# Optimization experiments

Hardware: AMD Instinct MI355X
Metric: run time of the kernel (lower is better)

Reference implementation:

```python
import jax, jax.numpy as jnp
import numpy as np
from jax import lax

SEGMENTS = 64
KERNEL = 5


def setup_inputs() -> dict:
    key = jax.random.key(0)
    k1, k2, k3 = jax.random.split(key, 3)
    B, S, F = 4, 4096, 1024
    A6 = 512 * 6
    inp = jax.random.normal(k1, (B, S, F), dtype=jnp.float32)
    W = jax.random.normal(k2, (A6, F), dtype=jnp.float32) * (1.0 / np.sqrt(F))
    b = jax.random.normal(k3, (A6,), dtype=jnp.float32) * 0.01
    return {"inp": inp, "W": W, "b": b}


def reference(inp, W, b):
    # Fused projection: [B,S,F] @ [F,6A] -> [B,S,6A]
    x = jnp.einsum('bsf,af->bsa', inp, W) + b
    qry, key, val, seg, loc, out = jnp.split(x, 6, axis=2)  # each [B,S,A]
    B, S, A = out.shape

    # Global aggregated attention branch
    agg = qry.mean(axis=1)                              # [B,A]
    scores = jnp.einsum('ba,bsa->bs', agg, key)         # [B,S]
    w = jax.nn.softmax(scores, axis=1)                  # [B,S]
    ctx = jnp.einsum('bs,bsa->ba', w, val)              # [B,A]
    aggregated = ctx[:, None, :] * out                  # [B,S,A]

    # Segment max-pool branch
    nseg = S // SEGMENTS
    seg4 = seg.reshape(B, nseg, SEGMENTS, A)
    seg_max = seg4.max(axis=2, keepdims=True)           # [B,nseg,1,A]
    segment_max_pooled = (seg_max * out.reshape(B, nseg, SEGMENTS, A)).reshape(B, S, A)

    # Local sliding-window max-pool branch (stride 1, pad KERNEL//2, -inf padding)
    pad = KERNEL // 2
    local_max_pooled = lax.reduce_window(
        loc, -jnp.inf, lax.max,
        window_dimensions=(1, KERNEL, 1),
        window_strides=(1, 1, 1),
        padding=((0, 0), (pad, pad), (0, 0)))           # [B,S,A]

    return aggregated + segment_max_pooled + local_max_pooled
```

## Files before the change

### kernel.cpp

```cpp
#include <hip/hip_runtime.h>
#include <hip/hip_bf16.h>
#include <stdint.h>

#define B_    4
#define S_    4096
#define F_    1024
#define A_    512
#define N3_   1536
#define M_    16384

#define BM    256
#define BN    192
#define BK    64
#define NT    (F_ / BK)

typedef __attribute__((ext_vector_type(8))) __bf16 bf16x8;
typedef __attribute__((ext_vector_type(4))) float  f32x4;

__device__ __forceinline__ float bflo(unsigned int u) {
  union { unsigned int i; float f; } v; v.i = u << 16; return v.f;
}
__device__ __forceinline__ float bfhi(unsigned int u) {
  union { unsigned int i; float f; } v; v.i = u & 0xffff0000u; return v.f;
}

__device__ __forceinline__ ushort4 cvt_bf4(float4 v) {
  ushort4 o;
  o.x = __builtin_bit_cast(unsigned short, __float2bfloat16(v.x));
  o.y = __builtin_bit_cast(unsigned short, __float2bfloat16(v.y));
  o.z = __builtin_bit_cast(unsigned short, __float2bfloat16(v.z));
  o.w = __builtin_bit_cast(unsigned short, __float2bfloat16(v.w));
  return o;
}

typedef __attribute__((address_space(3))) unsigned int lds_uint;
typedef const __attribute__((address_space(1))) unsigned int glob_uint;
__device__ __forceinline__ void lds_load16(const void* g, void* l) {
  __builtin_amdgcn_global_load_lds((glob_uint*)g, (lds_uint*)l, 16, 0, 0);
}

__global__ __launch_bounds__(256) void convert_mean_kernel(
    const float* __restrict__ inp, const float* __restrict__ W,
    unsigned short* __restrict__ inp_bf, unsigned short* __restrict__ w_bf,
    float* __restrict__ mu) {
  int blk = blockIdx.x;
  int t   = threadIdx.x;
  int r0  = blk * 32;
  int b   = r0 >> 12;
  float acc0 = 0.f, acc1 = 0.f, acc2 = 0.f, acc3 = 0.f;
  for (int r = 0; r < 32; r++) {
    size_t row = (size_t)(r0 + r);
    float4 v = ((const float4*)(inp + row * F_))[t];
    acc0 += v.x; acc1 += v.y; acc2 += v.z; acc3 += v.w;
    ((ushort4*)(inp_bf + row * F_))[t] = cvt_bf4(v);
  }
  atomicAdd(&mu[b * F_ + t * 4 + 0], acc0);
  atomicAdd(&mu[b * F_ + t * 4 + 1], acc1);
  atomicAdd(&mu[b * F_ + t * 4 + 2], acc2);
  atomicAdd(&mu[b * F_ + t * 4 + 3], acc3);

  const float* Wc = W + (size_t)N3_ * F_;
  const int n4 = (N3_ * F_) / 4;
  for (int i = blk * 256 + t; i < n4; i += 512 * 256) {
    ((ushort4*)w_bf)[i] = cvt_bf4(((const float4*)Wc)[i]);
  }
}

__global__ void agg_kernel(const float* __restrict__ mu, const float* __restrict__ W,
                           const float* __restrict__ bias, float* __restrict__ agg) {
  int gw = blockIdx.x * 4 + (threadIdx.x >> 6);
  int lane = threadIdx.x & 63;
  int b = gw >> 9, a = gw & 511;
  const float4* wr = (const float4*)(W + (size_t)a * F_);
  const float4* mr = (const float4*)(mu + b * F_);
  float s = 0.f;
#pragma unroll
  for (int k = 0; k < 4; k++) {
    float4 wv = wr[lane + 64 * k], mv = mr[lane + 64 * k];
    s += wv.x * mv.x + wv.y * mv.y + wv.z * mv.z + wv.w * mv.w;
  }
  for (int off = 32; off; off >>= 1) s += __shfl_down(s, off);
  if (lane == 0) agg[b * A_ + a] = s * (1.f / S_) + bias[a];
}

__global__ void v_kernel(const float* __restrict__ agg, const float* __restrict__ W,
                         const float* __restrict__ bias, float* __restrict__ v,
                         float* __restrict__ cvec) {
  int fc = blockIdx.x;
  int ac = blockIdx.y;
  int t = threadIdx.x;
  int f = fc * 256 + t;
  const float* Wk = W + (size_t)A_ * F_;
  float s0 = 0.f, s1 = 0.f, s2 = 0.f, s3 = 0.f;
  int a0 = ac * 64;
  for (int a = a0; a < a0 + 64; a++) {
    float wv = Wk[(size_t)a * F_ + f];
    s0 += agg[a] * wv;
    s1 += agg[A_ + a] * wv;
    s2 += agg[2 * A_ + a] * wv;
    s3 += agg[3 * A_ + a] * wv;
  }
  atomicAdd(&v[f], s0);
  atomicAdd(&v[F_ + f], s1);
  atomicAdd(&v[2 * F_ + f], s2);
  atomicAdd(&v[3 * F_ + f], s3);

  if (fc == 0 && ac == 0) {
    int bb = t >> 6, l = t & 63;
    float c = 0.f;
#pragma unroll
    for (int i = 0; i < 8; i++) c += agg[bb * A_ + l + 64 * i] * bias[A_ + l + 64 * i];
    for (int off = 32; off; off >>= 1) c += __shfl_down(c, off);
    if (l == 0) cvec[bb] = c;
  }
}

__global__ void scores_kernel(const unsigned short* __restrict__ inp_bf,
                              const float* __restrict__ v,
                              const float* __restrict__ cvec, float* __restrict__ scores) {
  int lane = threadIdx.x & 63;
  int row = blockIdx.x * 4 + (threadIdx.x >> 6);
  int b = row >> 12;
  const uint4* ip = (const uint4*)(inp_bf + (size_t)row * F_);
  const float4* vp = (const float4*)(v + b * F_);
  float s = 0.f;
#pragma unroll
  for (int k = 0; k < 2; k++) {
    uint4 x = ip[lane + 64 * k];
    float4 va = vp[(lane + 64 * k) * 2];
    float4 vb = vp[(lane + 64 * k) * 2 + 1];
    s += bflo(x.x) * va.x + bfhi(x.x) * va.y + bflo(x.y) * va.z + bfhi(x.y) * va.w +
         bflo(x.z) * vb.x + bfhi(x.z) * vb.y + bflo(x.w) * vb.z + bfhi(x.w) * vb.w;
  }
  for (int off = 32; off; off >>= 1) s += __shfl_down(s, off);
  if (lane == 0) scores[row] = s + cvec[b];
}

__global__ void softmax_kernel(float* __restrict__ sc) {
  __shared__ float red[256];
  int b = blockIdx.x, t = threadIdx.x;
  float* p = sc + b * S_;
  float vals[16];
  float m = -1e30f;
#pragma unroll
  for (int i = 0; i < 16; i++) { vals[i] = p[t + i * 256]; m = fmaxf(m, vals[i]); }
  red[t] = m; __syncthreads();
  for (int o = 128; o; o >>= 1) { if (t < o) red[t] = fmaxf(red[t], red[t + o]); __syncthreads(); }
  m = red[0]; __syncthreads();
  float sum = 0.f;
#pragma unroll
  for (int i = 0; i < 16; i++) { vals[i] = __expf(vals[i] - m); sum += vals[i]; }
  red[t] = sum; __syncthreads();
  for (int o = 128; o; o >>= 1) { if (t < o) red[t] += red[t + o]; __syncthreads(); }
  float inv = 1.f / red[0];
#pragma unroll
  for (int i = 0; i < 16; i++) p[t + i * 256] = vals[i] * inv;
}

__global__ void u_kernel(const unsigned short* __restrict__ inp_bf,
                         const float* __restrict__ w, float* __restrict__ u) {
  int b = blockIdx.z, fc = blockIdx.y, sc = blockIdx.x;
  int t = threadIdx.x;
  int f2 = fc * 512 + t * 2;
  int s0 = sc * 128;
  const float* wp = w + b * S_ + s0;
  const unsigned short* ip = inp_bf + ((size_t)(b * S_ + s0)) * F_ + f2;
  float a0 = 0.f, a1 = 0.f;
  for (int s = 0; s < 128; s++) {
    unsigned int xv = *(const unsigned int*)&ip[(size_t)s * F_];
    float ws = wp[s];
    a0 += ws * bflo(xv);
    a1 += ws * bfhi(xv);
  }
  atomicAdd(&u[b * F_ + f2], a0);
  atomicAdd(&u[b * F_ + f2 + 1], a1);
}

__global__ void ctx_kernel(const float* __restrict__ u, const float* __restrict__ W,
                           const float* __restrict__ bias, float* __restrict__ ctx) {
  int gw = blockIdx.x * 4 + (threadIdx.x >> 6);
  int lane = threadIdx.x & 63;
  int b = gw >> 9, a = gw & 511;
  const float4* wr = (const float4*)(W + (size_t)(2 * A_ + a) * F_);
  const float4* ur = (const float4*)(u + b * F_);
  float s = 0.f;
#pragma unroll
  for (int k = 0; k < 4; k++) {
    float4 wv = wr[lane + 64 * k], uv = ur[lane + 64 * k];
    s += wv.x * uv.x + wv.y * uv.y + wv.z * uv.z + wv.w * uv.w;
  }
  for (int off = 32; off; off >>= 1) s += __shfl_down(s, off);
  if (lane == 0) ctx[b * A_ + a] = s + bias[2 * A_ + a];
}

__global__ __launch_bounds__(512, 2) void gemm_kernel(
    const __hip_bfloat16* __restrict__ Abf,
    const __hip_bfloat16* __restrict__ Wbf,
    const float* __restrict__ bias,
    __hip_bfloat16* __restrict__ X) {
  extern __shared__ unsigned short smem[];
  unsigned short* ldsA = smem;
  unsigned short* ldsB = smem + 32768;

  int bid = blockIdx.x;
  int swz = (bid & 7) * 64 + (bid >> 3);
  int mb = swz >> 3;
  int nb = swz & 7;

  int tid  = threadIdx.x;
  int lane = tid & 63;
  int wv   = tid >> 6;
  int wm   = wv >> 2;
  int wn   = wv & 3;
  int lo   = lane & 15, hi = lane >> 4, sw = lane & 7;

  int bir0 = (((hi * 16)      ^ (sw << 4)) >> 1);
  int bir1 = (((64 + hi * 16) ^ (sw << 4)) >> 1);

  const __hip_bfloat16* Ab = Abf + (size_t)mb * BM * F_;
  const __hip_bfloat16* Bb = Wbf + (size_t)nb * BN * F_;

  int srow = tid >> 3;
  int sel  = ((tid & 7) ^ (srow & 7)) * 8;
  int ldst = wv * 512;

  f32x4 acc[8][3];
#pragma unroll
  for (int i = 0; i < 8; i++)
#pragma unroll
    for (int j = 0; j < 3; j++) acc[i][j] = (f32x4){0.f, 0.f, 0.f, 0.f};

  int aBase = (wm * 128 + lo) * 64;
  int bBase = (wn * 48 + lo) * 64;

#define STAGE(kt_, buf_)                                                                   \
  {                                                                                        \
    int kof_ = (kt_) * BK;                                                                 \
    unsigned short* la_ = ldsA + (buf_) * 16384;                                           \
    unsigned short* lb_ = ldsB + (buf_) * 12288;                                           \
    lds_load16(Ab + (size_t)(srow) * F_ + kof_ + sel,        la_ + 0 * 4096 + ldst);       \
    lds_load16(Ab + (size_t)(64 + srow) * F_ + kof_ + sel,   la_ + 1 * 4096 + ldst);       \
    lds_load16(Ab + (size_t)(128 + srow) * F_ + kof_ + sel,  la_ + 2 * 4096 + ldst);       \
    lds_load16(Ab + (size_t)(192 + srow) * F_ + kof_ + sel,  la_ + 3 * 4096 + ldst);       \
    lds_load16(Bb + (size_t)(srow) * F_ + kof_ + sel,        lb_ + 0 * 4096 + ldst);       \
    lds_load16(Bb + (size_t)(64 + srow) * F_ + kof_ + sel,   lb_ + 1 * 4096 + ldst);       \
    lds_load16(Bb + (size_t)(128 + srow) * F_ + kof_ + sel,  lb_ + 2 * 4096 + ldst);       \
  }

  STAGE(0, 0);

  for (int kt = 0; kt < NT; ++kt) {
    int c = kt & 1;
    __builtin_amdgcn_s_barrier();
    if (kt + 1 < NT) {
      STAGE(kt + 1, c ^ 1);
      asm volatile("s_waitcnt vmcnt(7)" ::: "memory");
    } else {
      asm volatile("s_waitcnt vmcnt(0)" ::: "memory");
    }
    __builtin_amdgcn_s_barrier();
    __builtin_amdgcn_sched_barrier(0);

    const unsigned short* la = ldsA + c * 16384;
    const unsigned short* lb = ldsB + c * 12288;

    bf16x8 aq[4][2], b01[2][2], b2[2];

#pragma unroll
    for (int i = 0; i < 4; i++) {
      aq[i][0] = *(const bf16x8*)&la[aBase + i * 1024 + bir0];
      aq[i][1] = *(const bf16x8*)&la[aBase + i * 1024 + bir1];
    }
#pragma unroll
    for (int j = 0; j < 2; j++) {
      b01[j][0] = *(const bf16x8*)&lb[bBase + j * 1024 + bir0];
      b01[j][1] = *(const bf16x8*)&lb[bBase + j * 1024 + bir1];
    }
    __builtin_amdgcn_s_setprio(1);
#pragma unroll
    for (int i = 0; i < 4; i++)
#pragma unroll
      for (int j = 0; j < 2; j++) {
        acc[i][j] = __builtin_amdgcn_mfma_f32_16x16x32_bf16(aq[i][0], b01[j][0], acc[i][j], 0, 0, 0);
        acc[i][j] = __builtin_amdgcn_mfma_f32_16x16x32_bf16(aq[i][1], b01[j][1], acc[i][j], 0, 0, 0);
      }
    __builtin_amdgcn_s_setprio(0);
    __builtin_amdgcn_sched_barrier(0);

    b2[0] = *(const bf16x8*)&lb[bBase + 2 * 1024 + bir0];
    b2[1] = *(const bf16x8*)&lb[bBase + 2 * 1024 + bir1];
    __builtin_amdgcn_s_setprio(1);
#pragma unroll
    for (int i = 0; i < 4; i++) {
      acc[i][2] = __builtin_amdgcn_mfma_f32_16x16x32_bf16(aq[i][0], b2[0], acc[i][2], 0, 0, 0);
      acc[i][2] = __builtin_amdgcn_mfma_f32_16x16x32_bf16(aq[i][1], b2[1], acc[i][2], 0, 0, 0);
    }
    __builtin_amdgcn_s_setprio(0);
    __builtin_amdgcn_sched_barrier(0);

#pragma unroll
    for (int i = 0; i < 4; i++) {
      aq[i][0] = *(const bf16x8*)&la[aBase + 4096 + i * 1024 + bir0];
      aq[i][1] = *(const bf16x8*)&la[aBase + 4096 + i * 1024 + bir1];
    }
    __builtin_amdgcn_s_setprio(1);
#pragma unroll
    for (int i = 0; i < 4; i++) {
      acc[4 + i][2] = __builtin_amdgcn_mfma_f32_16x16x32_bf16(aq[i][0], b2[0], acc[4 + i][2], 0, 0, 0);
      acc[4 + i][2] = __builtin_amdgcn_mfma_f32_16x16x32_bf16(aq[i][1], b2[1], acc[4 + i][2], 0, 0, 0);
    }
    __builtin_amdgcn_s_setprio(0);
    __builtin_amdgcn_sched_barrier(0);

    __builtin_amdgcn_s_setprio(1);
#pragma unroll
    for (int i = 0; i < 4; i++)
#pragma unroll
      for (int j = 0; j < 2; j++) {
        acc[4 + i][j] = __builtin_amdgcn_mfma_f32_16x16x32_bf16(aq[i][0], b01[j][0], acc[4 + i][j], 0, 0, 0);
        acc[4 + i][j] = __builtin_amdgcn_mfma_f32_16x16x32_bf16(aq[i][1], b01[j][1], acc[4 + i][j], 0, 0, 0);
      }
    __builtin_amdgcn_s_setprio(0);
    __builtin_amdgcn_sched_barrier(0);
  }
#undef STAGE

#pragma unroll
  for (int fm = 0; fm < 8; fm++) {
    int grow = mb * BM + wm * 128 + fm * 16 + hi * 4;
#pragma unroll
    for (int fn = 0; fn < 3; fn++) {
      int gcol = nb * BN + wn * 48 + fn * 16 + lo;
      float bv = bias[gcol];
#pragma unroll
      for (int rg = 0; rg < 4; rg++) {
        X[(size_t)(grow + rg) * N3_ + gcol] = __float2bfloat16(acc[fm][fn][rg] + bv);
      }
    }
  }
}

__global__ void final_kernel(const unsigned short* __restrict__ X,
                             const float* __restrict__ ctx,
                             float* __restrict__ out) {
  int b = blockIdx.y, seg = blockIdx.x;
  int t = threadIdx.x;
  int c0 = t * 2;
  int sbase = seg * 64;

  float m0 = -1e30f, m1 = -1e30f;
  size_t base = ((size_t)b * S_ + sbase) * N3_;
  for (int r = 0; r < 64; r++) {
    unsigned int sv = *(const unsigned int*)&X[base + (size_t)r * N3_ + c0];
    m0 = fmaxf(m0, bflo(sv));
    m1 = fmaxf(m1, bfhi(sv));
  }
  float2 cx = *(const float2*)&ctx[b * A_ + c0];
  float g0 = cx.x + m0, g1 = cx.y + m1;

  auto loadloc = [&](int s) -> unsigned int {
    if ((unsigned)s >= (unsigned)S_) return 0xFF80FF80u;
    return *(const unsigned int*)&X[((size_t)b * S_ + s) * N3_ + A_ + c0];
  };
  unsigned int w0 = loadloc(sbase - 2), w1 = loadloc(sbase - 1);
  unsigned int w2 = loadloc(sbase),     w3 = loadloc(sbase + 1);
  for (int rr = 0; rr < 64; rr++) {
    int s = sbase + rr;
    unsigned int w4 = loadloc(s + 2);
    float lo = fmaxf(fmaxf(fmaxf(bflo(w0), bflo(w1)), fmaxf(bflo(w2), bflo(w3))), bflo(w4));
    float hi = fmaxf(fmaxf(fmaxf(bfhi(w0), bfhi(w1)), fmaxf(bfhi(w2), bfhi(w3))), bfhi(w4));
    unsigned int ov = *(const unsigned int*)&X[((size_t)b * S_ + s) * N3_ + 2 * A_ + c0];
    float2 res;
    res.x = g0 * bflo(ov) + lo;
    res.y = g1 * bfhi(ov) + hi;
    *(float2*)&out[((size_t)b * S_ + s) * A_ + c0] = res;
    w0 = w1; w1 = w2; w2 = w3; w3 = w4;
  }
}

extern "C" void kernel_launch(void* const* d_in, const int* in_sizes, int n_in,
                              void* d_out, int out_size, void* d_ws, size_t ws_size,
                              hipStream_t stream) {
  const float* inp  = (const float*)d_in[0];
  const float* W    = (const float*)d_in[1];
  const float* bias = (const float*)d_in[2];
  float* out = (float*)d_out;
  char* ws = (char*)d_ws;

  const size_t X_OFF    = 0;
  const size_t INP_OFF  = 50331648;
  const size_t W_OFF    = 83886080;
  const size_t MU_OFF   = 87031808;
  const size_t U_OFF    = MU_OFF + 16384;
  const size_t V_OFF    = U_OFF + 16384;
  const size_t CV_OFF   = V_OFF + 16384;
  const size_t AGG_OFF  = CV_OFF + 256;
  const size_t CTX_OFF  = AGG_OFF + 8192;
  const size_t SC_OFF   = CTX_OFF + 8192;

  unsigned short* xbf    = (unsigned short*)(ws + X_OFF);
  unsigned short* inp_bf = (unsigned short*)(ws + INP_OFF);
  unsigned short* w_bf   = (unsigned short*)(ws + W_OFF);
  float* mu     = (float*)(ws + MU_OFF);
  float* u      = (float*)(ws + U_OFF);
  float* v      = (float*)(ws + V_OFF);
  float* cvec   = (float*)(ws + CV_OFF);
  float* agg    = (float*)(ws + AGG_OFF);
  float* ctx    = (float*)(ws + CTX_OFF);
  float* scores = (float*)(ws + SC_OFF);

  static int lds_attr_set = 0;
  (void)lds_attr_set;
  hipFuncSetAttribute(reinterpret_cast<const void*>(gemm_kernel),
                      hipFuncAttributeMaxDynamicSharedMemorySize, 114688);

  hipMemsetAsync(ws + MU_OFF, 0, 3 * 16384 + 256, stream);
  convert_mean_kernel<<<512, 256, 0, stream>>>(inp, W, inp_bf, w_bf, mu);
  gemm_kernel<<<512, 512, 114688, stream>>>((const __hip_bfloat16*)inp_bf,
                                            (const __hip_bfloat16*)w_bf,
                                            bias + 3 * A_, (__hip_bfloat16*)xbf);
  agg_kernel<<<512, 256, 0, stream>>>(mu, W, bias, agg);
  v_kernel<<<dim3(4, 8), 256, 0, stream>>>(agg, W, bias, v, cvec);
  scores_kernel<<<4096, 256, 0, stream>>>(inp_bf, v, cvec, scores);
  softmax_kernel<<<4, 256, 0, stream>>>(scores);
  u_kernel<<<dim3(32, 2, 4), 256, 0, stream>>>(inp_bf, scores, u);
  ctx_kernel<<<512, 256, 0, stream>>>(u, W, bias, ctx);
  final_kernel<<<dim3(64, 4), 256, 0, stream>>>(xbf, ctx, out);
}
```

Before: 151.3 us.

## Fuse pooling epilogue into GEMM and drop the intermediate X buffer

The GEMM now gives each block 64 columns from each of the seg, loc and out groups, so one block holds all three projections for its 256 rows. Segment max, the local sliding max and the final combine are computed in the epilogue through a transposed LDS tile, and fp32 output is written directly. This removes the bf16 X round trip through global memory and the separate final kernel. A small fixup kernel patches the sliding-window results at tile boundaries using side buffers, and the GEMM's warp tiling and load staging are reorganised.

```diff
diff --git a/kernel.cpp b/kernel.cpp
--- a/kernel.cpp
+++ b/kernel.cpp
@@ -10,9 +10,9 @@
 #define M_    16384
 
 #define BM    256
-#define BN    192
 #define BK    64
 #define NT    (F_ / BK)
+#define LDP   266
 
 typedef __attribute__((ext_vector_type(8))) __bf16 bf16x8;
 typedef __attribute__((ext_vector_type(4))) float  f32x4;
@@ -23,13 +23,16 @@
 __device__ __forceinline__ float bfhi(unsigned int u) {
   union { unsigned int i; float f; } v; v.i = u & 0xffff0000u; return v.f;
 }
+__device__ __forceinline__ float bf1(unsigned short u) {
+  union { unsigned int i; float f; } v; v.i = ((unsigned int)u) << 16; return v.f;
+}
+__device__ __forceinline__ unsigned short bfc(float f) {
+  return __builtin_bit_cast(unsigned short, __float2bfloat16(f));
+}
 
 __device__ __forceinline__ ushort4 cvt_bf4(float4 v) {
   ushort4 o;
-  o.x = __builtin_bit_cast(unsigned short, __float2bfloat16(v.x));
-  o.y = __builtin_bit_cast(unsigned short, __float2bfloat16(v.y));
-  o.z = __builtin_bit_cast(unsigned short, __float2bfloat16(v.z));
-  o.w = __builtin_bit_cast(unsigned short, __float2bfloat16(v.w));
+  o.x = bfc(v.x); o.y = bfc(v.y); o.z = bfc(v.z); o.w = bfc(v.w);
   return o;
 }
 
@@ -193,14 +196,19 @@
   if (lane == 0) ctx[b * A_ + a] = s + bias[2 * A_ + a];
 }
 
-__global__ __launch_bounds__(512, 2) void gemm_kernel(
+__global__ __launch_bounds__(512, 2) void gemm_fused(
     const __hip_bfloat16* __restrict__ Abf,
     const __hip_bfloat16* __restrict__ Wbf,
-    const float* __restrict__ bias,
-    __hip_bfloat16* __restrict__ X) {
+    const float* __restrict__ biasP,
+    const float* __restrict__ ctx,
+    float* __restrict__ out,
+    unsigned short* __restrict__ sideLoc,
+    float* __restrict__ sideGO) {
   extern __shared__ unsigned short smem[];
   unsigned short* ldsA = smem;
   unsigned short* ldsB = smem + 32768;
+  unsigned short* Xt   = smem;
+  float* segred = (float*)((char*)smem + 192 * LDP * 2);
 
   int bid = blockIdx.x;
   int swz = (bid & 7) * 64 + (bid >> 3);
@@ -210,171 +218,225 @@
   int tid  = threadIdx.x;
   int lane = tid & 63;
   int wv   = tid >> 6;
-  int wm   = wv >> 2;
-  int wn   = wv & 3;
+  int wm   = wv >> 1;
+  int wn   = wv & 1;
   int lo   = lane & 15, hi = lane >> 4, sw = lane & 7;
 
   int bir0 = (((hi * 16)      ^ (sw << 4)) >> 1);
   int bir1 = (((64 + hi * 16) ^ (sw << 4)) >> 1);
 
   const __hip_bfloat16* Ab = Abf + (size_t)mb * BM * F_;
-  const __hip_bfloat16* Bb = Wbf + (size_t)nb * BN * F_;
 
   int srow = tid >> 3;
   int sel  = ((tid & 7) ^ (srow & 7)) * 8;
   int ldst = wv * 512;
 
-  f32x4 acc[8][3];
-#pragma unroll
-  for (int i = 0; i < 8; i++)
-#pragma unroll
-    for (int j = 0; j < 3; j++) acc[i][j] = (f32x4){0.f, 0.f, 0.f, 0.f};
-
-  int aBase = (wm * 128 + lo) * 64;
-  int bBase = (wn * 48 + lo) * 64;
-
-#define STAGE(kt_, buf_)                                                                   \
-  {                                                                                        \
-    int kof_ = (kt_) * BK;                                                                 \
-    unsigned short* la_ = ldsA + (buf_) * 16384;                                           \
-    unsigned short* lb_ = ldsB + (buf_) * 12288;                                           \
-    lds_load16(Ab + (size_t)(srow) * F_ + kof_ + sel,        la_ + 0 * 4096 + ldst);       \
-    lds_load16(Ab + (size_t)(64 + srow) * F_ + kof_ + sel,   la_ + 1 * 4096 + ldst);       \
-    lds_load16(Ab + (size_t)(128 + srow) * F_ + kof_ + sel,  la_ + 2 * 4096 + ldst);       \
-    lds_load16(Ab + (size_t)(192 + srow) * F_ + kof_ + sel,  la_ + 3 * 4096 + ldst);       \
-    lds_load16(Bb + (size_t)(srow) * F_ + kof_ + sel,        lb_ + 0 * 4096 + ldst);       \
-    lds_load16(Bb + (size_t)(64 + srow) * F_ + kof_ + sel,   lb_ + 1 * 4096 + ldst);       \
-    lds_load16(Bb + (size_t)(128 + srow) * F_ + kof_ + sel,  lb_ + 2 * 4096 + ldst);       \
-  }
-
-  STAGE(0, 0);
+  f32x4 acc[4][6];
+#pragma unroll
+  for (int i = 0; i < 4; i++)
+#pragma unroll
+    for (int j = 0; j < 6; j++) acc[i][j] = (f32x4){0.f, 0.f, 0.f, 0.f};
+
+  int aBase = (wm * 64 + lo) * 64;
+  int bBase = (wn * 96 + lo) * 64;
+
+#define STG_A(kt_, buf_, r_)                                                              \
+  lds_load16(Ab + (size_t)((r_) * 64 + srow) * F_ + (kt_) * BK + sel,                     \
+             ldsA + (buf_) * 16384 + (r_) * 4096 + ldst)
+#define STG_B(kt_, buf_, q_)                                                              \
+  lds_load16(Wbf + (size_t)((q_) * 512 + nb * 64 + srow) * F_ + (kt_) * BK + sel,         \
+             ldsB + (buf_) * 12288 + (q_) * 4096 + ldst)
+
+  STG_A(0, 0, 0); STG_A(0, 0, 1); STG_A(0, 0, 2); STG_A(0, 0, 3);
+  STG_B(0, 0, 0); STG_B(0, 0, 1); STG_B(0, 0, 2);
 
   for (int kt = 0; kt < NT; ++kt) {
-    int c = kt & 1;
-    __builtin_amdgcn_s_barrier();
-    if (kt + 1 < NT) {
-      STAGE(kt + 1, c ^ 1);
-      asm volatile("s_waitcnt vmcnt(7)" ::: "memory");
+    int c = kt & 1, nx = c ^ 1;
+    bool pf = (kt + 1 < NT);
+    const unsigned short* la = ldsA + c * 16384;
+    const unsigned short* lb = ldsB + c * 12288;
+    bf16x8 af[4][2], bfr[2][2];
+
+    if (pf) {
+      STG_A(kt + 1, nx, 0); STG_A(kt + 1, nx, 1); STG_A(kt + 1, nx, 2);
+      asm volatile("s_waitcnt vmcnt(3)" ::: "memory");
     } else {
       asm volatile("s_waitcnt vmcnt(0)" ::: "memory");
     }
     __builtin_amdgcn_s_barrier();
+#pragma unroll
+    for (int i = 0; i < 4; i++) {
+      af[i][0] = *(const bf16x8*)&la[aBase + i * 1024 + bir0];
+      af[i][1] = *(const bf16x8*)&la[aBase + i * 1024 + bir1];
+    }
+#pragma unroll
+    for (int j = 0; j < 2; j++) {
+      bfr[j][0] = *(const bf16x8*)&lb[bBase + j * 1024 + bir0];
+      bfr[j][1] = *(const bf16x8*)&lb[bBase + j * 1024 + bir1];
+    }
+    asm volatile("s_waitcnt lgkmcnt(0)" ::: "memory");
     __builtin_amdgcn_sched_barrier(0);
-
-    const unsigned short* la = ldsA + c * 16384;
-    const unsigned short* lb = ldsB + c * 12288;
-
-    bf16x8 aq[4][2], b01[2][2], b2[2];
-
-#pragma unroll
-    for (int i = 0; i < 4; i++) {
-      aq[i][0] = *(const bf16x8*)&la[aBase + i * 1024 + bir0];
-      aq[i][1] = *(const bf16x8*)&la[aBase + i * 1024 + bir1];
-    }
-#pragma unroll
-    for (int j = 0; j < 2; j++) {
-      b01[j][0] = *(const bf16x8*)&lb[bBase + j * 1024 + bir0];
-      b01[j][1] = *(const bf16x8*)&lb[bBase + j * 1024 + bir1];
-    }
     __builtin_amdgcn_s_setprio(1);
 #pragma unroll
     for (int i = 0; i < 4; i++)
 #pragma unroll
       for (int j = 0; j < 2; j++) {
-        acc[i][j] = __builtin_amdgcn_mfma_f32_16x16x32_bf16(aq[i][0], b01[j][0], acc[i][j], 0, 0, 0);
-        acc[i][j] = __builtin_amdgcn_mfma_f32_16x16x32_bf16(aq[i][1], b01[j][1], acc[i][j], 0, 0, 0);
+        acc[i][j] = __builtin_amdgcn_mfma_f32_16x16x32_bf16(af[i][0], bfr[j][0], acc[i][j], 0, 0, 0);
+        acc[i][j] = __builtin_amdgcn_mfma_f32_16x16x32_bf16(af[i][1], bfr[j][1], acc[i][j], 0, 0, 0);
       }
     __builtin_amdgcn_s_setprio(0);
+    __builtin_amdgcn_s_barrier();
+
+#pragma unroll
+    for (int j = 0; j < 2; j++) {
+      bfr[j][0] = *(const bf16x8*)&lb[bBase + (2 + j) * 1024 + bir0];
+      bfr[j][1] = *(const bf16x8*)&lb[bBase + (2 + j) * 1024 + bir1];
+    }
+    if (pf) { STG_A(kt + 1, nx, 3); STG_B(kt + 1, nx, 0); }
+    __builtin_amdgcn_s_barrier();
+    asm volatile("s_waitcnt lgkmcnt(0)" ::: "memory");
     __builtin_amdgcn_sched_barrier(0);
-
-    b2[0] = *(const bf16x8*)&lb[bBase + 2 * 1024 + bir0];
-    b2[1] = *(const bf16x8*)&lb[bBase + 2 * 1024 + bir1];
     __builtin_amdgcn_s_setprio(1);
 #pragma unroll
-    for (int i = 0; i < 4; i++) {
-      acc[i][2] = __builtin_amdgcn_mfma_f32_16x16x32_bf16(aq[i][0], b2[0], acc[i][2], 0, 0, 0);
-      acc[i][2] = __builtin_amdgcn_mfma_f32_16x16x32_bf16(aq[i][1], b2[1], acc[i][2], 0, 0, 0);
-    }
-    __builtin_amdgcn_s_setprio(0);
-    __builtin_amdgcn_sched_barrier(0);
-
-#pragma unroll
-    for (int i = 0; i < 4; i++) {
-      aq[i][0] = *(const bf16x8*)&la[aBase + 4096 + i * 1024 + bir0];
-      aq[i][1] = *(const bf16x8*)&la[aBase + 4096 + i * 1024 + bir1];
-    }
-    __builtin_amdgcn_s_setprio(1);
-#pragma unroll
-    for (int i = 0; i < 4; i++) {
-      acc[4 + i][2] = __builtin_amdgcn_mfma_f32_16x16x32_bf16(aq[i][0], b2[0], acc[4 + i][2], 0, 0, 0);
-      acc[4 + i][2] = __builtin_amdgcn_mfma_f32_16x16x32_bf16(aq[i][1], b2[1], acc[4 + i][2], 0, 0, 0);
-    }
-    __builtin_amdgcn_s_setprio(0);
-    __builtin_amdgcn_sched_barrier(0);
-
-    __builtin_amdgcn_s_setprio(1);
-#pragma unroll
     for (int i = 0; i < 4; i++)
 #pragma unroll
       for (int j = 0; j < 2; j++) {
-        acc[4 + i][j] = __builtin_amdgcn_mfma_f32_16x16x32_bf16(aq[i][0], b01[j][0], acc[4 + i][j], 0, 0, 0);
-        acc[4 + i][j] = __builtin_amdgcn_mfma_f32_16x16x32_bf16(aq[i][1], b01[j][1], acc[4 + i][j], 0, 0, 0);
+        acc[i][2 + j] = __builtin_amdgcn_mfma_f32_16x16x32_bf16(af[i][0], bfr[j][0], acc[i][2 + j], 0, 0, 0);
+        acc[i][2 + j] = __builtin_amdgcn_mfma_f32_16x16x32_bf16(af[i][1], bfr[j][1], acc[i][2 + j], 0, 0, 0);
       }
     __builtin_amdgcn_s_setprio(0);
+    __builtin_amdgcn_s_barrier();
+
+#pragma unroll
+    for (int j = 0; j < 2; j++) {
+      bfr[j][0] = *(const bf16x8*)&lb[bBase + (4 + j) * 1024 + bir0];
+      bfr[j][1] = *(const bf16x8*)&lb[bBase + (4 + j) * 1024 + bir1];
+    }
+    if (pf) { STG_B(kt + 1, nx, 1); STG_B(kt + 1, nx, 2); }
+    __builtin_amdgcn_s_barrier();
+    asm volatile("s_waitcnt lgkmcnt(0)" ::: "memory");
     __builtin_amdgcn_sched_barrier(0);
-  }
-#undef STAGE
-
-#pragma unroll
-  for (int fm = 0; fm < 8; fm++) {
-    int grow = mb * BM + wm * 128 + fm * 16 + hi * 4;
-#pragma unroll
-    for (int fn = 0; fn < 3; fn++) {
-      int gcol = nb * BN + wn * 48 + fn * 16 + lo;
-      float bv = bias[gcol];
-#pragma unroll
-      for (int rg = 0; rg < 4; rg++) {
-        X[(size_t)(grow + rg) * N3_ + gcol] = __float2bfloat16(acc[fm][fn][rg] + bv);
+    __builtin_amdgcn_s_setprio(1);
+#pragma unroll
+    for (int i = 0; i < 4; i++)
+#pragma unroll
+      for (int j = 0; j < 2; j++) {
+        acc[i][4 + j] = __builtin_amdgcn_mfma_f32_16x16x32_bf16(af[i][0], bfr[j][0], acc[i][4 + j], 0, 0, 0);
+        acc[i][4 + j] = __builtin_amdgcn_mfma_f32_16x16x32_bf16(af[i][1], bfr[j][1], acc[i][4 + j], 0, 0, 0);
       }
-    }
-  }
-}
-
-__global__ void final_kernel(const unsigned short* __restrict__ X,
-                             const float* __restrict__ ctx,
+    __builtin_amdgcn_s_setprio(0);
+    __builtin_amdgcn_s_barrier();
+  }
+#undef STG_A
+#undef STG_B
+
+  float bias_r[6];
+#pragma unroll
+  for (int fj = 0; fj < 6; fj++) {
+    int cl = wn * 96 + fj * 16 + lo;
+    bias_r[fj] = biasP[(cl >> 6) * 512 + nb * 64 + (cl & 63)];
+  }
+#pragma unroll
+  for (int fi = 0; fi < 4; fi++) {
+#pragma unroll
+    for (int fj = 0; fj < 6; fj++) {
+      int cl = wn * 96 + fj * 16 + lo;
+      int r  = wm * 64 + fi * 16 + hi * 4;
+      float v0 = acc[fi][fj][0] + bias_r[fj];
+      float v1 = acc[fi][fj][1] + bias_r[fj];
+      float v2 = acc[fi][fj][2] + bias_r[fj];
+      float v3 = acc[fi][fj][3] + bias_r[fj];
+      unsigned int u01 = (unsigned int)bfc(v0) | ((unsigned int)bfc(v1) << 16);
+      unsigned int u23 = (unsigned int)bfc(v2) | ((unsigned int)bfc(v3) << 16);
+      *(unsigned int*)&Xt[cl * LDP + r]     = u01;
+      *(unsigned int*)&Xt[cl * LDP + r + 2] = u23;
+    }
+  }
+  __syncthreads();
+
+  if (tid < 256) {
+    int seg = tid >> 6, c = tid & 63;
+    int base = c * LDP + seg * 64;
+    float m = -1e30f;
+#pragma unroll
+    for (int k = 0; k < 32; k++) {
+      unsigned int u = *(const unsigned int*)&Xt[base + 2 * k];
+      m = fmaxf(m, fmaxf(bflo(u), bfhi(u)));
+    }
+    segred[seg * 64 + c] = m;
+  }
+  __syncthreads();
+
+  {
+    int c  = lane;
+    int r0 = wv * 32;
+    int b  = mb >> 4;
+    int gcol = nb * 64 + c;
+    float g = ctx[b * 512 + gcol] + segred[(r0 >> 6) * 64 + c];
+    int lbase = (64 + c) * LDP;
+    int obase = (128 + c) * LDP;
+    float lw0 = bf1(Xt[lbase + max(r0 - 2, 0)]);
+    float lw1 = bf1(Xt[lbase + max(r0 - 1, 0)]);
+    float lw2 = bf1(Xt[lbase + r0]);
+    float lw3 = bf1(Xt[lbase + r0 + 1]);
+    size_t obase_g = ((size_t)(mb * 256 + r0)) * 512 + gcol;
+#pragma unroll
+    for (int j = 0; j < 32; j++) {
+      int rn = min(r0 + j + 2, 255);
+      float lw4 = bf1(Xt[lbase + rn]);
+      float lm = fmaxf(fmaxf(fmaxf(lw0, lw1), fmaxf(lw2, lw3)), lw4);
+      float o = bf1(Xt[obase + r0 + j]);
+      out[obase_g + (size_t)j * 512] = g * o + lm;
+      lw0 = lw1; lw1 = lw2; lw2 = lw3; lw3 = lw4;
+    }
+  }
+
+  if (tid < 256) {
+    int rsel = tid >> 6, c = tid & 63;
+    int r = (rsel < 2) ? rsel : (252 + rsel);
+    int b = mb >> 4;
+    float g = ctx[b * 512 + nb * 64 + c] + segred[(r >> 6) * 64 + c];
+    float o = bf1(Xt[(128 + c) * LDP + r]);
+    int gr = mb * 4 + rsel;
+    sideLoc[gr * 512 + nb * 64 + c] = Xt[(64 + c) * LDP + r];
+    sideGO[gr * 512 + nb * 64 + c]  = g * o;
+  }
+}
+
+__global__ void fixup_kernel(const unsigned short* __restrict__ sideLoc,
+                             const float* __restrict__ sideGO,
                              float* __restrict__ out) {
-  int b = blockIdx.y, seg = blockIdx.x;
+  int rb = blockIdx.x;
+  int tb = rb & 15;
   int t = threadIdx.x;
-  int c0 = t * 2;
-  int sbase = seg * 64;
-
-  float m0 = -1e30f, m1 = -1e30f;
-  size_t base = ((size_t)b * S_ + sbase) * N3_;
-  for (int r = 0; r < 64; r++) {
-    unsigned int sv = *(const unsigned int*)&X[base + (size_t)r * N3_ + c0];
-    m0 = fmaxf(m0, bflo(sv));
-    m1 = fmaxf(m1, bfhi(sv));
-  }
-  float2 cx = *(const float2*)&ctx[b * A_ + c0];
-  float g0 = cx.x + m0, g1 = cx.y + m1;
-
-  auto loadloc = [&](int s) -> unsigned int {
-    if ((unsigned)s >= (unsigned)S_) return 0xFF80FF80u;
-    return *(const unsigned int*)&X[((size_t)b * S_ + s) * N3_ + A_ + c0];
-  };
-  unsigned int w0 = loadloc(sbase - 2), w1 = loadloc(sbase - 1);
-  unsigned int w2 = loadloc(sbase),     w3 = loadloc(sbase + 1);
-  for (int rr = 0; rr < 64; rr++) {
-    int s = sbase + rr;
-    unsigned int w4 = loadloc(s + 2);
-    float lo = fmaxf(fmaxf(fmaxf(bflo(w0), bflo(w1)), fmaxf(bflo(w2), bflo(w3))), bflo(w4));
-    float hi = fmaxf(fmaxf(fmaxf(bfhi(w0), bfhi(w1)), fmaxf(bfhi(w2), bfhi(w3))), bfhi(w4));
-    unsigned int ov = *(const unsigned int*)&X[((size_t)b * S_ + s) * N3_ + 2 * A_ + c0];
-    float2 res;
-    res.x = g0 * bflo(ov) + lo;
-    res.y = g1 * bfhi(ov) + hi;
-    *(float2*)&out[((size_t)b * S_ + s) * A_ + c0] = res;
-    w0 = w1; w1 = w2; w2 = w3; w3 = w4;
+  int rsel = t >> 6, cq = t & 63;
+#pragma unroll
+  for (int k = 0; k < 8; k++) {
+    int c = cq * 8 + k;
+    float miss;
+    int rl;
+    if (rsel == 0) {
+      if (tb == 0) continue;
+      miss = fmaxf(bf1(sideLoc[((rb - 1) * 4 + 2) * 512 + c]),
+                   bf1(sideLoc[((rb - 1) * 4 + 3) * 512 + c]));
+      rl = 0;
+    } else if (rsel == 1) {
+      if (tb == 0) continue;
+      miss = bf1(sideLoc[((rb - 1) * 4 + 3) * 512 + c]);
+      rl = 1;
+    } else if (rsel == 2) {
+      if (tb == 15) continue;
+      miss = bf1(sideLoc[((rb + 1) * 4 + 0) * 512 + c]);
+      rl = 254;
+    } else {
+      if (tb == 15) continue;
+      miss = fmaxf(bf1(sideLoc[((rb + 1) * 4 + 0) * 512 + c]),
+                   bf1(sideLoc[((rb + 1) * 4 + 1) * 512 + c]));
+      rl = 255;
+    }
+    size_t oi = ((size_t)rb * 256 + rl) * 512 + c;
+    float cand = sideGO[(rb * 4 + rsel) * 512 + c] + miss;
+    out[oi] = fmaxf(out[oi], cand);
   }
 }
 
@@ -387,18 +449,18 @@
   float* out = (float*)d_out;
   char* ws = (char*)d_ws;
 
-  const size_t X_OFF    = 0;
-  const size_t INP_OFF  = 50331648;
-  const size_t W_OFF    = 83886080;
-  const size_t MU_OFF   = 87031808;
+  const size_t INP_OFF  = 0;
+  const size_t W_OFF    = 33554432;
+  const size_t MU_OFF   = 36700160;
   const size_t U_OFF    = MU_OFF + 16384;
   const size_t V_OFF    = U_OFF + 16384;
   const size_t CV_OFF   = V_OFF + 16384;
   const size_t AGG_OFF  = CV_OFF + 256;
   const size_t CTX_OFF  = AGG_OFF + 8192;
   const size_t SC_OFF   = CTX_OFF + 8192;
-
-  unsigned short* xbf    = (unsigned short*)(ws + X_OFF);
+  const size_t SL_OFF   = SC_OFF + 65536;
+  const size_t SG_OFF   = SL_OFF + 262144;
+
   unsigned short* inp_bf = (unsigned short*)(ws + INP_OFF);
   unsigned short* w_bf   = (unsigned short*)(ws + W_OFF);
   float* mu     = (float*)(ws + MU_OFF);
@@ -408,22 +470,22 @@
   float* agg    = (float*)(ws + AGG_OFF);
   float* ctx    = (float*)(ws + CTX_OFF);
   float* scores = (float*)(ws + SC_OFF);
-
-  static int lds_attr_set = 0;
-  (void)lds_attr_set;
-  hipFuncSetAttribute(reinterpret_cast<const void*>(gemm_kernel),
+  unsigned short* sideLoc = (unsigned short*)(ws + SL_OFF);
+  float* sideGO = (float*)(ws + SG_OFF);
+
+  hipFuncSetAttribute(reinterpret_cast<const void*>(gemm_fused),
                       hipFuncAttributeMaxDynamicSharedMemorySize, 114688);
 
   hipMemsetAsync(ws + MU_OFF, 0, 3 * 16384 + 256, stream);
   convert_mean_kernel<<<512, 256, 0, stream>>>(inp, W, inp_bf, w_bf, mu);
-  gemm_kernel<<<512, 512, 114688, stream>>>((const __hip_bfloat16*)inp_bf,
-                                            (const __hip_bfloat16*)w_bf,
-                                            bias + 3 * A_, (__hip_bfloat16*)xbf);
   agg_kernel<<<512, 256, 0, stream>>>(mu, W, bias, agg);
   v_kernel<<<dim3(4, 8), 256, 0, stream>>>(agg, W, bias, v, cvec);
   scores_kernel<<<4096, 256, 0, stream>>>(inp_bf, v, cvec, scores);
   softmax_kernel<<<4, 256, 0, stream>>>(scores);
   u_kernel<<<dim3(32, 2, 4), 256, 0, stream>>>(inp_bf, scores, u);
   ctx_kernel<<<512, 256, 0, stream>>>(u, W, bias, ctx);
-  final_kernel<<<dim3(64, 4), 256, 0, stream>>>(xbf, ctx, out);
-}
+  gemm_fused<<<512, 512, 114688, stream>>>((const __hip_bfloat16*)inp_bf,
+                                           (const __hip_bfloat16*)w_bf,
+                                           bias + 3 * A_, ctx, out, sideLoc, sideGO);
+  fixup_kernel<<<64, 256, 0, stream>>>(sideLoc, sideGO, out);
+}
```

After: 128.1 us. 15.3% less time.
